# Kernel optimization log

Measured on AMD Instinct MI355X. Metric: run time of the kernel, lower is better.

Reference implementation:

```python
import jax, jax.numpy as jnp
import numpy as np

HEADS = 16
DIM_HEAD = 64
LN_EPS = 1e-5


def setup_inputs() -> dict:
    key = jax.random.key(0)
    ks = jax.random.split(key, 4)
    b, n, dim = 2, 2048, 1024
    inner = HEADS * DIM_HEAD
    x = jax.random.normal(ks[0], (b, n, dim), dtype=jnp.float32)
    gamma = jnp.ones((dim,), dtype=jnp.float32)
    beta = jnp.zeros((dim,), dtype=jnp.float32)
    w_qkv = jax.random.normal(ks[1], (dim, 3 * inner), dtype=jnp.float32) * (dim ** -0.5)
    w_out = jax.random.normal(ks[2], (inner, dim), dtype=jnp.float32) * (inner ** -0.5)
    b_out = jnp.zeros((dim,), dtype=jnp.float32)
    return {"x": x, "gamma": gamma, "beta": beta, "w_qkv": w_qkv, "w_out": w_out, "b_out": b_out}


def reference(x, gamma, beta, w_qkv, w_out, b_out):
    b, n, dim = x.shape
    h, d = HEADS, DIM_HEAD
    scale = d ** -0.5
    # LayerNorm
    mu = jnp.mean(x, axis=-1, keepdims=True)
    var = jnp.mean(jnp.square(x - mu), axis=-1, keepdims=True)
    xn = (x - mu) * jax.lax.rsqrt(var + LN_EPS) * gamma + beta
    # QKV projection (no bias)
    qkv = xn @ w_qkv  # [b, n, 3*h*d]
    q, k, v = jnp.split(qkv, 3, axis=-1)
    split_heads = lambda t: t.reshape(b, n, h, d).transpose(0, 2, 1, 3)  # [b, h, n, d]
    q, k, v = split_heads(q), split_heads(k), split_heads(v)
    q = q * scale
    sim = jnp.einsum('bhid,bhjd->bhij', q, k)  # full O(n^2) score matrix
    attn = jax.nn.softmax(sim, axis=-1)
    out = jnp.einsum('bhij,bhjd->bhid', attn, v)
    out = out.transpose(0, 2, 1, 3).reshape(b, n, h * d)
    return out @ w_out + b_out
```

## Files before the change

kernel.cpp:

```cpp
#include <hip/hip_runtime.h>
#include <hip/hip_bf16.h>

#define HEADS 16
#define DH 64
#define DIM 1024
#define SEQ 2048
#define BATCH 2
#define ROWS (BATCH*SEQ)
#define NQKV (3*DIM)
#define NKVT (SEQ/64)
#define NSPLIT 2
#define QSCALE 0.18033688011112042f
#define NBH (BATCH*HEADS)
#define NQROWS (NBH*SEQ)

typedef __attribute__((ext_vector_type(8))) short bf16x8;
typedef __attribute__((ext_vector_type(4))) float f32x4;
typedef __attribute__((ext_vector_type(16))) float f32x16;
typedef __attribute__((ext_vector_type(4))) unsigned u32x4;
typedef __hip_bfloat16 bf16;

static __device__ __forceinline__ bf16 f2bf(float v){ return __float2bfloat16(v); }

static __device__ __forceinline__ unsigned pack2bf(float a, float b){
  bf16 x = f2bf(a), y = f2bf(b);
  unsigned short ux = *(unsigned short*)&x, uy = *(unsigned short*)&y;
  return (unsigned)ux | ((unsigned)uy << 16);
}

static __device__ __forceinline__ void gload16(const void* g, void* lds){
  __builtin_amdgcn_global_load_lds((const __attribute__((address_space(1))) void*)g,
                                   (__attribute__((address_space(3))) void*)lds, 16, 0, 0);
}

__global__ __launch_bounds__(256) void ln_kernel(const float* __restrict__ x,
    const float* __restrict__ gamma, const float* __restrict__ beta,
    bf16* __restrict__ xn)
{
  int row = blockIdx.x;
  int tid = threadIdx.x;
  float4 v = ((const float4*)(x + (size_t)row*DIM))[tid];
  float s  = v.x+v.y+v.z+v.w;
  float ss = v.x*v.x+v.y*v.y+v.z*v.z+v.w*v.w;
  #pragma unroll
  for (int m=1;m<64;m<<=1){ s += __shfl_xor(s,m); ss += __shfl_xor(ss,m); }
  __shared__ float red[8];
  int wid = tid>>6;
  if ((tid&63)==0){ red[wid]=s; red[4+wid]=ss; }
  __syncthreads();
  s  = red[0]+red[1]+red[2]+red[3];
  ss = red[4]+red[5]+red[6]+red[7];
  float mu  = s*(1.0f/DIM);
  float var = ss*(1.0f/DIM) - mu*mu;
  float inv = rsqrtf(var + 1e-5f);
  float4 g  = ((const float4*)gamma)[tid];
  float4 bb = ((const float4*)beta)[tid];
  __align__(8) bf16 o[4];
  o[0]=f2bf((v.x-mu)*inv*g.x+bb.x);
  o[1]=f2bf((v.y-mu)*inv*g.y+bb.y);
  o[2]=f2bf((v.z-mu)*inv*g.z+bb.z);
  o[3]=f2bf((v.w-mu)*inv*g.w+bb.w);
  *(uint2*)&xn[(size_t)row*DIM + tid*4] = *(const uint2*)o;
}

__global__ __launch_bounds__(256) void transpose_cast(const float* __restrict__ in,
    bf16* __restrict__ out, int R, int C)
{
  __shared__ __align__(16) bf16 t[64][72];
  int c0 = blockIdx.x*64, r0 = blockIdx.y*64;
  int tid = threadIdx.x;
  int row = tid>>2;
  int cq  = (tid&3)*16;
  #pragma unroll
  for (int j=0;j<4;j++){
    float4 v = *(const float4*)&in[(size_t)(r0+row)*C + c0 + cq + j*4];
    t[cq+j*4+0][row] = f2bf(v.x);
    t[cq+j*4+1][row] = f2bf(v.y);
    t[cq+j*4+2][row] = f2bf(v.z);
    t[cq+j*4+3][row] = f2bf(v.w);
  }
  __syncthreads();
  int c = tid>>2; int rq = (tid&3)*16;
  uint4 u0 = *(const uint4*)&t[c][rq];
  uint4 u1 = *(const uint4*)&t[c][rq+8];
  *(uint4*)&out[(size_t)(c0+c)*R + r0 + rq]     = u0;
  *(uint4*)&out[(size_t)(c0+c)*R + r0 + rq + 8] = u1;
}

__global__ __launch_bounds__(256) void gemm_bt(
    const bf16* __restrict__ A, const bf16* __restrict__ Bt, int K, int mode,
    bf16* __restrict__ qb, bf16* __restrict__ kb, bf16* __restrict__ vtb,
    float* __restrict__ outf, const float* __restrict__ bias)
{
  __shared__ __align__(16) bf16 aL[128*64];
  __shared__ __align__(16) bf16 bL[128*64];
  int tid = threadIdx.x;
  int w = tid>>6, l = tid&63;
  int lr = l&15, lh = l>>4;
  int wr = w>>1, wc = w&1;
  int by = blockIdx.y, bx = blockIdx.x;
  const bf16* Ab = A  + (size_t)(by*128)*K;
  const bf16* Bb = Bt + (size_t)(bx*128)*K;
  int scol = ((l&7)*8) ^ ((l>>3)<<3);
  int frsw = (lr&7)<<3;
  f32x4 acc[4][4] = {};
  for (int k0=0; k0<K; k0+=64){
    #pragma unroll
    for (int i=0;i<4;i++){
      int row = w*32 + i*8;
      gload16(Ab + (size_t)(row + (l>>3))*K + k0 + scol, aL + row*64);
      gload16(Bb + (size_t)(row + (l>>3))*K + k0 + scol, bL + row*64);
    }
    __syncthreads();
    #pragma unroll
    for (int kk=0;kk<2;kk++){
      bf16x8 af[4], bfr[4];
      #pragma unroll
      for (int m=0;m<4;m++) af[m]  = *(const bf16x8*)&aL[(wr*64 + m*16 + lr)*64 + ((kk*32 + lh*8) ^ frsw)];
      #pragma unroll
      for (int n=0;n<4;n++) bfr[n] = *(const bf16x8*)&bL[(wc*64 + n*16 + lr)*64 + ((kk*32 + lh*8) ^ frsw)];
      #pragma unroll
      for (int m=0;m<4;m++)
        #pragma unroll
        for (int n=0;n<4;n++)
          acc[m][n] = __builtin_amdgcn_mfma_f32_16x16x32_bf16(af[m], bfr[n], acc[m][n], 0,0,0);
    }
    __syncthreads();
  }
  int rb = by*128 + wr*64, cb = bx*128 + wc*64;
  if (mode == 1){
    #pragma unroll
    for (int m=0;m<4;m++)
      #pragma unroll
      for (int n=0;n<4;n++)
        #pragma unroll
        for (int reg=0;reg<4;reg++){
          int r = rb + m*16 + lh*4 + reg;
          int c = cb + n*16 + lr;
          outf[(size_t)r*DIM + c] = acc[m][n][reg] + bias[c];
        }
  } else if (bx < 8){
    int b = rb >> 11;
    int nn0 = rb & 2047;
    #pragma unroll
    for (int m=0;m<4;m++)
      #pragma unroll
      for (int n=0;n<4;n++)
        #pragma unroll
        for (int reg=0;reg<4;reg++){
          int nn = nn0 + m*16 + lh*4 + reg;
          int c  = cb + n*16 + lr;
          int hh = c >> 6, dd = c & 63;
          qb[((size_t)(b*HEADS + hh)*SEQ + nn)*DH + dd] = f2bf(acc[m][n][reg]*QSCALE);
        }
  } else if (bx < 16){
    int b = rb >> 11;
    int kvt = (rb & 2047) >> 6;
    int hh0 = ((cb - 1024) >> 6);
    #pragma unroll
    for (int m=0;m<4;m++)
      #pragma unroll
      for (int reg=0;reg<4;reg++){
        int kvi = m*16 + lh*4 + reg;
        int sw  = (kvi&7)<<3;
        #pragma unroll
        for (int n=0;n<4;n++){
          int dd = n*16 + lr;
          kb[((size_t)(b*HEADS + hh0)*NKVT + kvt)*4096 + kvi*64 + (dd ^ sw)] = f2bf(acc[m][n][reg]);
        }
      }
  } else {
    bf16* tl = (w < 2 ? aL : bL) + (w&1)*4096;
    int b   = rb >> 11;
    int kvt = (rb & 2047) >> 6;
    int hh  = (cb - 2048) >> 6;
    #pragma unroll
    for (int n=0;n<4;n++){
      int dd = n*16 + lr;
      int sw = (dd&7)<<3;
      #pragma unroll
      for (int m=0;m<4;m++)
        #pragma unroll
        for (int reg=0;reg<4;reg++)
          tl[dd*64 + ((m*16 + lh*4 + reg) ^ sw)] = f2bf(acc[m][n][reg]);
    }
    __syncthreads();
    size_t gb = ((size_t)(b*HEADS + hh)*NKVT + kvt)*4096;
    #pragma unroll
    for (int j=0;j<8;j++)
      *(uint4*)&vtb[gb + j*512 + l*8] = *(const uint4*)&tl[j*512 + l*8];
  }
}

__global__ __launch_bounds__(256,4) void attn_part(
    const bf16* __restrict__ qb, const bf16* __restrict__ kb,
    const bf16* __restrict__ vtb,
    float* __restrict__ Opart, float* __restrict__ Mpart, float* __restrict__ Spart)
{
  __shared__ __align__(16) bf16 Kl[2][4096];
  __shared__ __align__(16) bf16 Vl[2][4096];
  int tid = threadIdx.x;
  int w = tid>>6, l = tid&63;
  int q5 = l & 31;
  int hi = l >> 5;
  int swz = (q5&7)<<3;
  int bh = blockIdx.y;
  int sp = blockIdx.z;
  int ts = sp*16, te = ts+16;
  const bf16* Q  = qb  + (size_t)bh*SEQ*DH;
  const bf16* Kt = kb  + (size_t)bh*NKVT*4096;
  const bf16* Vt = vtb + (size_t)bh*NKVT*4096;
  int q0w = blockIdx.x*128 + w*32;

  bf16x8 qf[4];
  #pragma unroll
  for (int st=0;st<4;st++)
    qf[st] = *(const bf16x8*)&Q[(size_t)(q0w + q5)*DH + st*16 + hi*8];

  f32x16 o0 = {}, o1 = {};
  float mrun = -3e38f, lrun = 0.f;

  {
    const bf16* ks = Kt + (size_t)ts*4096;
    const bf16* vs = Vt + (size_t)ts*4096;
    gload16(ks + w*1024       + l*8, &Kl[0][w*1024      ]);
    gload16(ks + w*1024 + 512 + l*8, &Kl[0][w*1024 + 512]);
    gload16(vs + w*1024       + l*8, &Vl[0][w*1024      ]);
    gload16(vs + w*1024 + 512 + l*8, &Vl[0][w*1024 + 512]);
  }

  for (int t=ts; t<te; t++){
    int cur = (t-ts)&1;
    __syncthreads();
    if (t+1 < te){
      const bf16* ks = Kt + (size_t)(t+1)*4096;
      const bf16* vs = Vt + (size_t)(t+1)*4096;
      gload16(ks + w*1024       + l*8, &Kl[cur^1][w*1024      ]);
      gload16(ks + w*1024 + 512 + l*8, &Kl[cur^1][w*1024 + 512]);
      gload16(vs + w*1024       + l*8, &Vl[cur^1][w*1024      ]);
      gload16(vs + w*1024 + 512 + l*8, &Vl[cur^1][w*1024 + 512]);
    }
    f32x16 s0 = {}, s1 = {};
    __builtin_amdgcn_s_setprio(1);
    #pragma unroll
    for (int st=0;st<4;st++){
      bf16x8 kf0 = *(const bf16x8*)&Kl[cur][(q5     )*64 + ((st*16 + hi*8) ^ swz)];
      bf16x8 kf1 = *(const bf16x8*)&Kl[cur][(32 + q5)*64 + ((st*16 + hi*8) ^ swz)];
      s0 = __builtin_amdgcn_mfma_f32_32x32x16_bf16(kf0, qf[st], s0, 0,0,0);
      s1 = __builtin_amdgcn_mfma_f32_32x32x16_bf16(kf1, qf[st], s1, 0,0,0);
    }
    __builtin_amdgcn_s_setprio(0);
    float pm = -3e38f;
    #pragma unroll
    for (int r=0;r<16;r++) pm = fmaxf(pm, fmaxf(s0[r], s1[r]));
    pm = fmaxf(pm, __shfl_xor(pm, 32));
    if (__any(pm > mrun + 8.f)){
      float mn = fmaxf(mrun, pm);
      float sc = __builtin_amdgcn_exp2f(mrun - mn);
      mrun = mn;
      lrun *= sc;
      #pragma unroll
      for (int reg=0;reg<16;reg++){
        float scr = __shfl(sc, (l & 32) | ((reg&3) + 8*(reg>>2) + 4*hi));
        o0[reg] *= scr;
        o1[reg] *= scr;
      }
    }
    float rs = 0.f;
    #pragma unroll
    for (int r=0;r<16;r++){
      float p0 = __builtin_amdgcn_exp2f(s0[r] - mrun); s0[r] = p0; rs += p0;
      float p1 = __builtin_amdgcn_exp2f(s1[r] - mrun); s1[r] = p1; rs += p1;
    }
    rs += __shfl_xor(rs, 32);
    lrun += rs;
    #define PV_STEP(SV, SGN)                                                         \
    {                                                                                \
      unsigned Aw = pack2bf(SV[SGN+0], SV[SGN+1]);                                   \
      unsigned Bw = pack2bf(SV[SGN+2], SV[SGN+3]);                                   \
      unsigned Cw = pack2bf(SV[SGN+4], SV[SGN+5]);                                   \
      unsigned Dw = pack2bf(SV[SGN+6], SV[SGN+7]);                                   \
      asm volatile("v_permlane32_swap_b32 %0, %1" : "+v"(Aw), "+v"(Cw));             \
      asm volatile("v_permlane32_swap_b32 %0, %1" : "+v"(Bw), "+v"(Dw));             \
      u32x4 pw = {Aw, Bw, Cw, Dw};                                                   \
      bf16x8 pa = *(const bf16x8*)&pw;                                               \
      bf16x8 vf0 = *(const bf16x8*)&Vl[cur][(q5     )*64 + ((kvs*16 + hi*8) ^ swz)]; \
      bf16x8 vf1 = *(const bf16x8*)&Vl[cur][(32 + q5)*64 + ((kvs*16 + hi*8) ^ swz)]; \
      __builtin_amdgcn_s_setprio(1);                                                 \
      o0 = __builtin_amdgcn_mfma_f32_32x32x16_bf16(pa, vf0, o0, 0,0,0);              \
      o1 = __builtin_amdgcn_mfma_f32_32x32x16_bf16(pa, vf1, o1, 0,0,0);              \
      __builtin_amdgcn_s_setprio(0);                                                 \
    }
    { int kvs = 0; PV_STEP(s0, 0) }
    { int kvs = 1; PV_STEP(s0, 8) }
    { int kvs = 2; PV_STEP(s1, 0) }
    { int kvs = 3; PV_STEP(s1, 8) }
    #undef PV_STEP
  }
  size_t rbase = ((size_t)sp*NBH + bh)*SEQ;
  #pragma unroll
  for (int reg=0;reg<16;reg++){
    int q = q0w + (reg&3) + 8*(reg>>2) + 4*hi;
    Opart[(rbase + q)*64 + q5]      = o0[reg];
    Opart[(rbase + q)*64 + 32 + q5] = o1[reg];
  }
  if (l < 32){
    Mpart[rbase + q0w + l] = mrun;
    Spart[rbase + q0w + l] = lrun;
  }
}

__global__ __launch_bounds__(256) void attn_merge(
    const float* __restrict__ Opart, const float* __restrict__ Mpart,
    const float* __restrict__ Spart, bf16* __restrict__ ao)
{
  int r = blockIdx.x*4 + (threadIdx.x>>6);
  int d = threadIdx.x & 63;
  float m0 = Mpart[r], m1 = Mpart[NQROWS + r];
  float m  = fmaxf(m0, m1);
  float c0 = exp2f(m0 - m), c1 = exp2f(m1 - m);
  float denom = Spart[r]*c0 + Spart[NQROWS + r]*c1;
  float v = Opart[(size_t)r*64 + d]*c0
          + Opart[((size_t)NQROWS + r)*64 + d]*c1;
  int bh = r >> 11, q = r & 2047;
  int b = bh >> 4, h = bh & 15;
  ao[((size_t)(b*SEQ + q))*DIM + h*DH + d] = f2bf(v / denom);
}

extern "C" void kernel_launch(void* const* d_in, const int* in_sizes, int n_in,
                              void* d_out, int out_size, void* d_ws, size_t ws_size,
                              hipStream_t stream)
{
  const float* x     = (const float*)d_in[0];
  const float* gamma = (const float*)d_in[1];
  const float* beta  = (const float*)d_in[2];
  const float* w_qkv = (const float*)d_in[3];
  const float* w_out = (const float*)d_in[4];
  const float* b_out = (const float*)d_in[5];
  float* out = (float*)d_out;

  bf16* ws  = (bf16*)d_ws;
  bf16* xn  = ws;
  bf16* wqt = xn  + (size_t)ROWS*DIM;
  bf16* wot = wqt + (size_t)NQKV*DIM;
  bf16* qb  = wot + (size_t)DIM*DIM;
  bf16* kb  = qb  + (size_t)NBH*SEQ*DH;
  bf16* vtb = kb  + (size_t)NBH*SEQ*DH;
  bf16* ao  = vtb + (size_t)NBH*SEQ*DH;
  float* Opart = (float*)(ao + (size_t)ROWS*DIM);
  float* Mpart = Opart + (size_t)NSPLIT*NQROWS*DH;
  float* Spart = Mpart + (size_t)NSPLIT*NQROWS;

  hipLaunchKernelGGL(ln_kernel, dim3(ROWS), dim3(256), 0, stream, x, gamma, beta, xn);
  hipLaunchKernelGGL(transpose_cast, dim3(NQKV/64, DIM/64), dim3(256), 0, stream, w_qkv, wqt, DIM, NQKV);
  hipLaunchKernelGGL(transpose_cast, dim3(DIM/64,  DIM/64), dim3(256), 0, stream, w_out, wot, DIM, DIM);
  hipLaunchKernelGGL(gemm_bt, dim3(NQKV/128, ROWS/128), dim3(256), 0, stream,
                     xn, wqt, DIM, 0, qb, kb, vtb, (float*)nullptr, (const float*)nullptr);
  hipLaunchKernelGGL(attn_part, dim3(SEQ/128, NBH, NSPLIT), dim3(256), 0, stream,
                     qb, kb, vtb, Opart, Mpart, Spart);
  hipLaunchKernelGGL(attn_merge, dim3(NQROWS/4), dim3(256), 0, stream,
                     Opart, Mpart, Spart, ao);
  hipLaunchKernelGGL(gemm_bt, dim3(DIM/128, ROWS/128), dim3(256), 0, stream,
                     ao, wot, DIM, 1, (bf16*)nullptr, (bf16*)nullptr, (bf16*)nullptr, out, b_out);
}
```

Measured before the change: 145.2 us.

## Compute softmax row sums via MFMA with ones vector and use packed bf16 convert

Replaces the VALU row-sum reduction and cross-lane shuffle with an extra MFMA against a vector of bf16 ones, accumulating the denominator in a third accumulator that is rescaled alongside the output. It also switches the float-to-bf16 packing to the native v_cvt_pk_bf16_f32 instruction and precomputes the swizzled LDS offsets. This trades VALU work for 50% more MFMA work per step and another 16 accumulator registers, and the denominator is now summed from bf16-rounded probabilities.

```diff
diff --git a/kernel.cpp b/kernel.cpp
--- a/kernel.cpp
+++ b/kernel.cpp
@@ -26,6 +26,12 @@
   bf16 x = f2bf(a), y = f2bf(b);
   unsigned short ux = *(unsigned short*)&x, uy = *(unsigned short*)&y;
   return (unsigned)ux | ((unsigned)uy << 16);
+}
+
+static __device__ __forceinline__ unsigned cvtpk(float a, float b){
+  unsigned r;
+  asm("v_cvt_pk_bf16_f32 %0, %1, %2" : "=v"(r) : "v"(a), "v"(b));
+  return r;
 }
 
 static __device__ __forceinline__ void gload16(const void* g, void* lds){
@@ -212,13 +218,22 @@
   const bf16* Vt = vtb + (size_t)bh*NKVT*4096;
   int q0w = blockIdx.x*128 + w*32;
 
+  int co[4];
+  #pragma unroll
+  for (int st=0;st<4;st++) co[st] = (st*16 + hi*8) ^ swz;
+  int r0 = q5*64, r1 = r0 + 2048;
+
   bf16x8 qf[4];
   #pragma unroll
   for (int st=0;st<4;st++)
     qf[st] = *(const bf16x8*)&Q[(size_t)(q0w + q5)*DH + st*16 + hi*8];
 
-  f32x16 o0 = {}, o1 = {};
-  float mrun = -3e38f, lrun = 0.f;
+  bf16x8 vone;
+  #pragma unroll
+  for (int i=0;i<8;i++) vone[i] = (short)0x3f80;
+
+  f32x16 o0 = {}, o1 = {}, osum = {};
+  float mrun = -3e38f;
 
   {
     const bf16* ks = Kt + (size_t)ts*4096;
@@ -244,8 +259,8 @@
     __builtin_amdgcn_s_setprio(1);
     #pragma unroll
     for (int st=0;st<4;st++){
-      bf16x8 kf0 = *(const bf16x8*)&Kl[cur][(q5     )*64 + ((st*16 + hi*8) ^ swz)];
-      bf16x8 kf1 = *(const bf16x8*)&Kl[cur][(32 + q5)*64 + ((st*16 + hi*8) ^ swz)];
+      bf16x8 kf0 = *(const bf16x8*)&Kl[cur][r0 + co[st]];
+      bf16x8 kf1 = *(const bf16x8*)&Kl[cur][r1 + co[st]];
       s0 = __builtin_amdgcn_mfma_f32_32x32x16_bf16(kf0, qf[st], s0, 0,0,0);
       s1 = __builtin_amdgcn_mfma_f32_32x32x16_bf16(kf1, qf[st], s1, 0,0,0);
     }
@@ -258,43 +273,41 @@
       float mn = fmaxf(mrun, pm);
       float sc = __builtin_amdgcn_exp2f(mrun - mn);
       mrun = mn;
-      lrun *= sc;
       #pragma unroll
       for (int reg=0;reg<16;reg++){
         float scr = __shfl(sc, (l & 32) | ((reg&3) + 8*(reg>>2) + 4*hi));
         o0[reg] *= scr;
         o1[reg] *= scr;
+        osum[reg] *= scr;
       }
     }
-    float rs = 0.f;
     #pragma unroll
     for (int r=0;r<16;r++){
-      float p0 = __builtin_amdgcn_exp2f(s0[r] - mrun); s0[r] = p0; rs += p0;
-      float p1 = __builtin_amdgcn_exp2f(s1[r] - mrun); s1[r] = p1; rs += p1;
-    }
-    rs += __shfl_xor(rs, 32);
-    lrun += rs;
-    #define PV_STEP(SV, SGN)                                                         \
+      s0[r] = __builtin_amdgcn_exp2f(s0[r] - mrun);
+      s1[r] = __builtin_amdgcn_exp2f(s1[r] - mrun);
+    }
+    #define PV_STEP(SV, SGN, KVS)                                                    \
     {                                                                                \
-      unsigned Aw = pack2bf(SV[SGN+0], SV[SGN+1]);                                   \
-      unsigned Bw = pack2bf(SV[SGN+2], SV[SGN+3]);                                   \
-      unsigned Cw = pack2bf(SV[SGN+4], SV[SGN+5]);                                   \
-      unsigned Dw = pack2bf(SV[SGN+6], SV[SGN+7]);                                   \
+      unsigned Aw = cvtpk(SV[SGN+0], SV[SGN+1]);                                     \
+      unsigned Bw = cvtpk(SV[SGN+2], SV[SGN+3]);                                     \
+      unsigned Cw = cvtpk(SV[SGN+4], SV[SGN+5]);                                     \
+      unsigned Dw = cvtpk(SV[SGN+6], SV[SGN+7]);                                     \
       asm volatile("v_permlane32_swap_b32 %0, %1" : "+v"(Aw), "+v"(Cw));             \
       asm volatile("v_permlane32_swap_b32 %0, %1" : "+v"(Bw), "+v"(Dw));             \
       u32x4 pw = {Aw, Bw, Cw, Dw};                                                   \
       bf16x8 pa = *(const bf16x8*)&pw;                                               \
-      bf16x8 vf0 = *(const bf16x8*)&Vl[cur][(q5     )*64 + ((kvs*16 + hi*8) ^ swz)]; \
-      bf16x8 vf1 = *(const bf16x8*)&Vl[cur][(32 + q5)*64 + ((kvs*16 + hi*8) ^ swz)]; \
+      bf16x8 vf0 = *(const bf16x8*)&Vl[cur][r0 + co[KVS]];                           \
+      bf16x8 vf1 = *(const bf16x8*)&Vl[cur][r1 + co[KVS]];                           \
       __builtin_amdgcn_s_setprio(1);                                                 \
       o0 = __builtin_amdgcn_mfma_f32_32x32x16_bf16(pa, vf0, o0, 0,0,0);              \
       o1 = __builtin_amdgcn_mfma_f32_32x32x16_bf16(pa, vf1, o1, 0,0,0);              \
+      osum = __builtin_amdgcn_mfma_f32_32x32x16_bf16(pa, vone, osum, 0,0,0);         \
       __builtin_amdgcn_s_setprio(0);                                                 \
     }
-    { int kvs = 0; PV_STEP(s0, 0) }
-    { int kvs = 1; PV_STEP(s0, 8) }
-    { int kvs = 2; PV_STEP(s1, 0) }
-    { int kvs = 3; PV_STEP(s1, 8) }
+    PV_STEP(s0, 0, 0)
+    PV_STEP(s0, 8, 1)
+    PV_STEP(s1, 0, 2)
+    PV_STEP(s1, 8, 3)
     #undef PV_STEP
   }
   size_t rbase = ((size_t)sp*NBH + bh)*SEQ;
@@ -304,9 +317,14 @@
     Opart[(rbase + q)*64 + q5]      = o0[reg];
     Opart[(rbase + q)*64 + 32 + q5] = o1[reg];
   }
-  if (l < 32){
+  if (l < 32)
     Mpart[rbase + q0w + l] = mrun;
-    Spart[rbase + q0w + l] = lrun;
+  if (q5 == 0){
+    #pragma unroll
+    for (int reg=0;reg<16;reg++){
+      int q = q0w + (reg&3) + 8*(reg>>2) + 4*hi;
+      Spart[rbase + q] = osum[reg];
+    }
   }
 }
 
```

Result: faster. 142.4 us (-2.0%).
